# Performance work log

Measured on AMD Instinct MI355X. Metric: run time of the kernel, lower is better.

Reference implementation:

```python
import jax, jax.numpy as jnp
import numpy as np

B, NQ, NKV = 2, 2048, 2048
DIM, CTX_DIM = 1024, 1024
HEADS, DIM_HEAD = 16, 64
INNER = HEADS * DIM_HEAD  # 1024
SCALE = DIM_HEAD ** -0.5


def setup_inputs() -> dict:
    key = jax.random.key(0)
    ks = jax.random.split(key, 6)
    x = jax.random.normal(ks[0], (B, NQ, DIM), dtype=jnp.float32)
    context = jax.random.normal(ks[1], (B, NKV, CTX_DIM), dtype=jnp.float32)
    # nn.Linear weights stored as [out, in] in torch; we keep [in, out] for x @ W.
    Wq = jax.random.normal(ks[2], (DIM, INNER), dtype=jnp.float32) / np.sqrt(DIM)
    Wkv = jax.random.normal(ks[3], (CTX_DIM, 2 * INNER), dtype=jnp.float32) / np.sqrt(CTX_DIM)
    Wout = jax.random.normal(ks[4], (INNER, DIM), dtype=jnp.float32) / np.sqrt(INNER)
    bout = jax.random.normal(ks[5], (DIM,), dtype=jnp.float32) * 0.01
    return {"x": x, "context": context, "Wq": Wq, "Wkv": Wkv, "Wout": Wout, "bout": bout}


def reference(x, context, Wq, Wkv, Wout, bout):
    q = x @ Wq                      # [B, Nq, inner]
    kv = context @ Wkv              # [B, Nkv, 2*inner]
    k, v = jnp.split(kv, 2, axis=-1)

    def split_heads(t):             # [B, N, inner] -> [B, H, N, dh]
        return t.reshape(t.shape[0], t.shape[1], HEADS, DIM_HEAD).transpose(0, 2, 1, 3)

    q, k, v = split_heads(q), split_heads(k), split_heads(v)
    dots = jnp.einsum('bhqd,bhkd->bhqk', q, k) * SCALE  # [B, H, Nq, Nkv]
    attn = jax.nn.softmax(dots, axis=-1)
    out = jnp.einsum('bhqk,bhkd->bhqd', attn, v)        # [B, H, Nq, dh]
    out = out.transpose(0, 2, 1, 3).reshape(out.shape[0], out.shape[2], INNER)
    return out @ Wout + bout        # [B, Nq, dim]
```

## Files before the change

### kernel.cpp

```cpp
#include <hip/hip_runtime.h>
#include <hip/hip_bf16.h>
#include <stdint.h>

#define NQ 2048
#define NKV 2048
#define DIM 1024
#define INNER 1024
#define HEADS 16
#define DH 64
#define BATCH 2

typedef float f32x4 __attribute__((ext_vector_type(4)));
typedef float f32x16 __attribute__((ext_vector_type(16)));
typedef __bf16 bf16x8 __attribute__((ext_vector_type(8)));
typedef unsigned int u32x4 __attribute__((ext_vector_type(4)));

__device__ inline ushort f2b(float f) {
    uint32_t u = __builtin_bit_cast(uint32_t, f);
    u += 0x7fff + ((u >> 16) & 1);
    return (ushort)(u >> 16);
}

__device__ inline uint pkbf16(float lo, float hi) {
    __hip_bfloat162 h = __float22bfloat162_rn(make_float2(lo, hi));
    uint r;
    __builtin_memcpy(&r, &h, 4);
    return r;
}

__device__ __forceinline__ void gload16(const void* g, void* lds) {
    __builtin_amdgcn_global_load_lds(
        (const __attribute__((address_space(1))) unsigned int*)g,
        (__attribute__((address_space(3))) unsigned int*)lds, 16, 0, 0);
}

__global__ void prep(const float* __restrict__ x, const float* __restrict__ ctx,
                     const float* __restrict__ Wq, const float* __restrict__ Wkv,
                     const float* __restrict__ Wout,
                     ushort* __restrict__ xb, ushort* __restrict__ cb,
                     ushort* __restrict__ Wqt, ushort* __restrict__ Wkvt,
                     ushort* __restrict__ Woutt) {
    int z = blockIdx.z;
    if (z < 4) {
        __shared__ ushort tile[32][33];
        const float* src; ushort* dst; int C;
        if (z == 0)      { src = Wq;          dst = Wqt;                C = 1024; }
        else if (z == 1) { src = Wkv;         dst = Wkvt;               C = 2048; }
        else if (z == 2) { src = Wkv + 1024;  dst = Wkvt + 1024 * 1024; C = 2048; }
        else             { src = Wout;        dst = Woutt;              C = 1024; }
        int c0 = blockIdx.x * 32, r0 = blockIdx.y * 32;
        int tx = threadIdx.x, ty = threadIdx.y;
#pragma unroll
        for (int i = 0; i < 4; i++)
            tile[ty + i * 8][tx] = f2b(src[(size_t)(r0 + ty + i * 8) * C + c0 + tx]);
        __syncthreads();
#pragma unroll
        for (int i = 0; i < 4; i++)
            dst[(size_t)(c0 + ty + i * 8) * 1024 + r0 + tx] = tile[tx][ty + i * 8];
    } else {
        const int n4 = (BATCH * NQ * DIM) / 4;
        int fb = blockIdx.y * 32 + blockIdx.x;
        int t = threadIdx.y * 32 + threadIdx.x;
        for (int i = fb * 256 + t; i < 2 * n4; i += 1024 * 256) {
            float4 v;
            if (i < n4) v = ((const float4*)x)[i];
            else        v = ((const float4*)ctx)[i - n4];
            ushort4 o;
            o.x = f2b(v.x); o.y = f2b(v.y); o.z = f2b(v.z); o.w = f2b(v.w);
            if (i < n4) ((ushort4*)xb)[i] = o;
            else        ((ushort4*)cb)[i - n4] = o;
        }
    }
}

__global__ __launch_bounds__(256) void gemm_qkv(const ushort* __restrict__ xb, const ushort* __restrict__ cb,
                                                const ushort* __restrict__ Wqt, const ushort* __restrict__ Wkvt,
                                                ushort* __restrict__ qb, ushort* __restrict__ kb,
                                                ushort* __restrict__ vtb, float qscale) {
    constexpr int K = 1024, NT = 32;
    __shared__ ushort lds[24576];
    int flat = blockIdx.x;
    int swz = (flat & 7) * 96 + (flat >> 3);
    bool isq = swz < 256;
    const ushort *A, *Bt;
    int m0, n0;
    if (isq) { A = xb; Bt = Wqt;  m0 = (swz >> 3) * 128;  n0 = (swz & 7) * 128; }
    else     { int b2 = swz - 256; A = cb; Bt = Wkvt; m0 = (b2 >> 4) * 128; n0 = (b2 & 15) * 128; }
    int t = threadIdx.x, l = t & 63, w = t >> 6;
    int wr = w >> 1, wc = w & 1;
    int lg = l >> 4, lc = l & 15;
    f32x4 acc[4][4] = {};

    auto stage = [&](int buf, int k0) {
#pragma unroll
        for (int i = 0; i < 2; i++) {
            int s = w + i * 4;
            gload16(A + (size_t)(m0 + (s & 1) * 64 + l) * K + k0 + (s >> 1) * 8, &lds[buf * 8192 + s * 512]);
            gload16(Bt + (size_t)(n0 + (s & 1) * 64 + l) * K + k0 + (s >> 1) * 8, &lds[buf * 8192 + 4096 + s * 512]);
        }
    };

    stage(0, 0);
    stage(1, 32);
    for (int tt = 0; tt < NT; ++tt) {
        int cur = tt % 3;
        if (tt + 2 < NT) {
            stage((tt + 2) % 3, (tt + 2) * 32);
            asm volatile("s_waitcnt vmcnt(8)" ::: "memory");
        } else if (tt + 1 < NT) {
            asm volatile("s_waitcnt vmcnt(4)" ::: "memory");
        } else {
            asm volatile("s_waitcnt vmcnt(0)" ::: "memory");
        }
        __builtin_amdgcn_s_barrier();
        asm volatile("" ::: "memory");
        bf16x8 af[4], bf[4];
#pragma unroll
        for (int mi = 0; mi < 4; mi++)
            af[mi] = *(const bf16x8*)&lds[cur * 8192 + (lg * 128 + wr * 64 + mi * 16 + lc) * 8];
#pragma unroll
        for (int ni = 0; ni < 4; ni++)
            bf[ni] = *(const bf16x8*)&lds[cur * 8192 + 4096 + (lg * 128 + wc * 64 + ni * 16 + lc) * 8];
        __builtin_amdgcn_s_setprio(1);
#pragma unroll
        for (int mi = 0; mi < 4; mi++)
#pragma unroll
            for (int ni = 0; ni < 4; ni++)
                acc[mi][ni] = __builtin_amdgcn_mfma_f32_16x16x32_bf16(af[mi], bf[ni], acc[mi][ni], 0, 0, 0);
        __builtin_amdgcn_s_setprio(0);
        asm volatile("s_waitcnt lgkmcnt(0)" ::: "memory");
        __builtin_amdgcn_s_barrier();
        asm volatile("" ::: "memory");
    }
    if (isq) {
#pragma unroll
        for (int mi = 0; mi < 4; mi++)
#pragma unroll
            for (int ni = 0; ni < 4; ni++)
#pragma unroll
                for (int r = 0; r < 4; r++) {
                    int m = m0 + wr * 64 + mi * 16 + lg * 4 + r;
                    int n = n0 + wc * 64 + ni * 16 + lc;
                    qb[(size_t)m * 1024 + n] = f2b(acc[mi][ni][r] * qscale);
                }
    } else if (n0 < 1024) {
#pragma unroll
        for (int mi = 0; mi < 4; mi++)
#pragma unroll
            for (int ni = 0; ni < 4; ni++)
#pragma unroll
                for (int r = 0; r < 4; r++) {
                    int m = m0 + wr * 64 + mi * 16 + lg * 4 + r;
                    int n = n0 + wc * 64 + ni * 16 + lc;
                    kb[(size_t)m * 1024 + n] = f2b(acc[mi][ni][r]);
                }
    } else {
        int b = m0 >> 11, kv0 = m0 & 2047;
        int h0 = (n0 - 1024) >> 6;
#pragma unroll
        for (int mi = 0; mi < 4; mi++)
#pragma unroll
            for (int ni = 0; ni < 4; ni++)
#pragma unroll
                for (int r = 0; r < 4; r++) {
                    int ml = wr * 64 + mi * 16 + lg * 4 + r;
                    int nl = wc * 64 + ni * 16 + lc;
                    lds[nl * 136 + ml] = f2b(acc[mi][ni][r]);
                }
        __syncthreads();
#pragma unroll
        for (int c = 0; c < 8; c++) {
            int idx = c * 256 + t;
            int rrow = idx >> 4;
            int chunk = idx & 15;
            int h = h0 + (rrow >> 6), d = rrow & 63;
            u32x4 v = *(u32x4*)&lds[rrow * 136 + chunk * 8];
            *(u32x4*)&vtb[(((size_t)b * HEADS + h) * DH + d) * (size_t)NKV + kv0 + chunk * 8] = v;
        }
    }
}

__global__ __launch_bounds__(256) void gemm_out(const ushort* __restrict__ A, const ushort* __restrict__ Bt,
                                                float* __restrict__ C0, const float* __restrict__ bias) {
    constexpr int K = 1024, NT = 32;
    __shared__ ushort lds[24576];
    int flat = blockIdx.x;
    int swz = (flat & 7) * 32 + (flat >> 3);
    int m0 = (swz >> 3) * 128, n0 = (swz & 7) * 128;
    int t = threadIdx.x, l = t & 63, w = t >> 6;
    int wr = w >> 1, wc = w & 1;
    int lg = l >> 4, lc = l & 15;
    f32x4 acc[4][4] = {};

    auto stage = [&](int buf, int k0) {
#pragma unroll
        for (int i = 0; i < 2; i++) {
            int s = w + i * 4;
            gload16(A + (size_t)(m0 + (s & 1) * 64 + l) * K + k0 + (s >> 1) * 8, &lds[buf * 8192 + s * 512]);
            gload16(Bt + (size_t)(n0 + (s & 1) * 64 + l) * K + k0 + (s >> 1) * 8, &lds[buf * 8192 + 4096 + s * 512]);
        }
    };

    stage(0, 0);
    stage(1, 32);
    for (int tt = 0; tt < NT; ++tt) {
        int cur = tt % 3;
        if (tt + 2 < NT) {
            stage((tt + 2) % 3, (tt + 2) * 32);
            asm volatile("s_waitcnt vmcnt(8)" ::: "memory");
        } else if (tt + 1 < NT) {
            asm volatile("s_waitcnt vmcnt(4)" ::: "memory");
        } else {
            asm volatile("s_waitcnt vmcnt(0)" ::: "memory");
        }
        __builtin_amdgcn_s_barrier();
        asm volatile("" ::: "memory");
        bf16x8 af[4], bf[4];
#pragma unroll
        for (int mi = 0; mi < 4; mi++)
            af[mi] = *(const bf16x8*)&lds[cur * 8192 + (lg * 128 + wr * 64 + mi * 16 + lc) * 8];
#pragma unroll
        for (int ni = 0; ni < 4; ni++)
            bf[ni] = *(const bf16x8*)&lds[cur * 8192 + 4096 + (lg * 128 + wc * 64 + ni * 16 + lc) * 8];
        __builtin_amdgcn_s_setprio(1);
#pragma unroll
        for (int mi = 0; mi < 4; mi++)
#pragma unroll
            for (int ni = 0; ni < 4; ni++)
                acc[mi][ni] = __builtin_amdgcn_mfma_f32_16x16x32_bf16(af[mi], bf[ni], acc[mi][ni], 0, 0, 0);
        __builtin_amdgcn_s_setprio(0);
        asm volatile("s_waitcnt lgkmcnt(0)" ::: "memory");
        __builtin_amdgcn_s_barrier();
        asm volatile("" ::: "memory");
    }
#pragma unroll
    for (int mi = 0; mi < 4; mi++)
#pragma unroll
        for (int ni = 0; ni < 4; ni++)
#pragma unroll
            for (int r = 0; r < 4; r++) {
                int m = m0 + wr * 64 + mi * 16 + lg * 4 + r;
                int n = n0 + wc * 64 + ni * 16 + lc;
                C0[(size_t)m * 1024 + n] = acc[mi][ni][r] + bias[n];
            }
}

__global__ __launch_bounds__(256, 3) void attn9(const ushort* __restrict__ qb, const ushort* __restrict__ kb,
                                                const ushort* __restrict__ vtb, ushort* __restrict__ ob) {
    __shared__ ushort Ks[3][4096];
    __shared__ ushort Vs[3][4096];
    int flat = blockIdx.x;
    int swz = (flat & 7) * 64 + (flat >> 3);
    int qt = swz & 15, h = (swz >> 4) & 15, b = swz >> 8;
    int t = threadIdx.x, l = t & 63, w = t >> 6;
    int ll = l & 31, hi = l >> 5;
    const ushort* Qg = qb + (size_t)b * NQ * INNER + h * DH;
    const ushort* Kg = kb + (size_t)b * NKV * INNER + h * DH;
    const ushort* Vg = vtb + (((size_t)b * HEADS + h) * DH) * NKV;
    int q0 = qt * 128;
    constexpr int NT2 = NKV / 64;

    bf16x8 qf[4];
#pragma unroll
    for (int dchunk = 0; dchunk < 4; dchunk++) {
        int dc = dchunk * 2 + hi;
        qf[dchunk] = *(const bf16x8*)&Qg[(size_t)(q0 + w * 32 + ll) * INNER + dc * 8];
    }
    auto stageKV = [&](int buf, int kv0) {
#pragma unroll
        for (int i = 0; i < 2; i++) {
            int s = w + i * 4;
            gload16(Kg + (size_t)(kv0 + l) * INNER + s * 8, &Ks[buf][s * 512]);
            gload16(Vg + (size_t)l * NKV + kv0 + s * 8, &Vs[buf][s * 512]);
        }
    };
    stageKV(0, 0);
    stageKV(1, 64);

    f32x16 o0 = {}, o1 = {};
    float m_ = -1e30f, s_ = 0.f;
    f32x16 zf = {};

    for (int tt = 0; tt < NT2; ++tt) {
        int cur = tt % 3;
        if (tt == 0) {
            asm volatile("s_waitcnt vmcnt(4)" ::: "memory");
        } else if (tt + 1 < NT2) {
            asm volatile("s_waitcnt vmcnt(4)" ::: "memory");
        } else {
            asm volatile("s_waitcnt vmcnt(0)" ::: "memory");
        }
        __builtin_amdgcn_s_barrier();
        asm volatile("" ::: "memory");
        if (tt + 2 < NT2) stageKV((tt + 2) % 3, (tt + 2) * 64);

        f32x16 st0 = zf, st1 = zf;
        __builtin_amdgcn_s_setprio(1);
#pragma unroll
        for (int dchunk = 0; dchunk < 4; dchunk++) {
            int dc = dchunk * 2 + hi;
            bf16x8 kf0 = *(const bf16x8*)&Ks[cur][(dc * 64 + ll) * 8];
            bf16x8 kf1 = *(const bf16x8*)&Ks[cur][(dc * 64 + 32 + ll) * 8];
            st0 = __builtin_amdgcn_mfma_f32_32x32x16_bf16(kf0, qf[dchunk], st0, 0, 0, 0);
            st1 = __builtin_amdgcn_mfma_f32_32x32x16_bf16(kf1, qf[dchunk], st1, 0, 0, 0);
        }
        __builtin_amdgcn_s_setprio(0);

        float mx;
        {
            f32x16 m01 = __builtin_elementwise_max(st0, st1);
            float a = fmaxf(fmaxf(m01[0], m01[1]), fmaxf(m01[2], m01[3]));
            float b2 = fmaxf(fmaxf(m01[4], m01[5]), fmaxf(m01[6], m01[7]));
            float c = fmaxf(fmaxf(m01[8], m01[9]), fmaxf(m01[10], m01[11]));
            float d = fmaxf(fmaxf(m01[12], m01[13]), fmaxf(m01[14], m01[15]));
            mx = fmaxf(fmaxf(a, b2), fmaxf(c, d));
        }
        mx = fmaxf(mx, __shfl_xor(mx, 32));
        if (!__all(mx - m_ <= 8.f)) {
            float mn2 = fmaxf(m_, mx);
            float fac = __builtin_amdgcn_exp2f(m_ - mn2);
            m_ = mn2; s_ *= fac; o0 *= fac; o1 *= fac;
        }
        float mn = m_;
#pragma unroll
        for (int r = 0; r < 16; r++) st0[r] = __builtin_amdgcn_exp2f(st0[r] - mn);
#pragma unroll
        for (int r = 0; r < 16; r++) st1[r] = __builtin_amdgcn_exp2f(st1[r] - mn);
        float rs;
        {
            f32x16 sm = st0 + st1;
            float a = (sm[0] + sm[1]) + (sm[2] + sm[3]);
            float b2 = (sm[4] + sm[5]) + (sm[6] + sm[7]);
            float c = (sm[8] + sm[9]) + (sm[10] + sm[11]);
            float d = (sm[12] + sm[13]) + (sm[14] + sm[15]);
            rs = (a + b2) + (c + d);
        }
        rs += __shfl_xor(rs, 32);
        s_ += rs;

        bf16x8 pb[4];
#pragma unroll
        for (int kvb = 0; kvb < 2; kvb++)
#pragma unroll
            for (int c = 0; c < 2; c++) {
                int base = c * 8;
                const f32x16& s0 = (kvb == 0) ? st0 : st1;
                uint a0 = pkbf16(s0[base + 0], s0[base + 1]);
                uint a1 = pkbf16(s0[base + 2], s0[base + 3]);
                uint b0 = pkbf16(s0[base + 4], s0[base + 5]);
                uint b1 = pkbf16(s0[base + 6], s0[base + 7]);
                asm volatile("v_permlane32_swap_b32 %0, %1" : "+v"(a0), "+v"(b0));
                asm volatile("v_permlane32_swap_b32 %0, %1" : "+v"(a1), "+v"(b1));
                u32x4 wrd = {a0, a1, b0, b1};
                pb[kvb * 2 + c] = __builtin_bit_cast(bf16x8, wrd);
            }

        __builtin_amdgcn_s_setprio(1);
#pragma unroll
        for (int kvchunk = 0; kvchunk < 4; kvchunk++) {
            int kvc = kvchunk * 2 + hi;
            bf16x8 vf0 = *(const bf16x8*)&Vs[cur][(kvc * 64 + ll) * 8];
            bf16x8 vf1 = *(const bf16x8*)&Vs[cur][(kvc * 64 + 32 + ll) * 8];
            o0 = __builtin_amdgcn_mfma_f32_32x32x16_bf16(vf0, pb[kvchunk], o0, 0, 0, 0);
            o1 = __builtin_amdgcn_mfma_f32_32x32x16_bf16(vf1, pb[kvchunk], o1, 0, 0, 0);
        }
        __builtin_amdgcn_s_setprio(0);
    }

    ushort* Og = ob + (size_t)b * NQ * INNER + h * DH;
    float inv = 1.f / s_;
    int q = q0 + w * 32 + ll;
#pragma unroll
    for (int rq = 0; rq < 4; rq++) {
        int d0 = 8 * rq + 4 * hi;
        uint2 pw;
        pw.x = pkbf16(o0[4 * rq + 0] * inv, o0[4 * rq + 1] * inv);
        pw.y = pkbf16(o0[4 * rq + 2] * inv, o0[4 * rq + 3] * inv);
        *(uint2*)&Og[(size_t)q * INNER + d0] = pw;
        uint2 pw1;
        pw1.x = pkbf16(o1[4 * rq + 0] * inv, o1[4 * rq + 1] * inv);
        pw1.y = pkbf16(o1[4 * rq + 2] * inv, o1[4 * rq + 3] * inv);
        *(uint2*)&Og[(size_t)q * INNER + 32 + d0] = pw1;
    }
}

extern "C" void kernel_launch(void* const* d_in, const int* in_sizes, int n_in,
                              void* d_out, int out_size, void* d_ws, size_t ws_size,
                              hipStream_t stream) {
    const float* x    = (const float*)d_in[0];
    const float* ctx  = (const float*)d_in[1];
    const float* Wq   = (const float*)d_in[2];
    const float* Wkv  = (const float*)d_in[3];
    const float* Wout = (const float*)d_in[4];
    const float* bout = (const float*)d_in[5];
    float* out = (float*)d_out;

    if (ws_size < (size_t)(56u << 20)) return;
    char* ws = (char*)d_ws;
    ushort* xb    = (ushort*)(ws);
    ushort* cb    = (ushort*)(ws + (8u << 20));
    ushort* ob    = (ushort*)(ws + (8u << 20));
    ushort* qb    = (ushort*)(ws + (16u << 20));
    ushort* kb    = (ushort*)(ws + (24u << 20));
    ushort* vtb   = (ushort*)(ws + (32u << 20));
    ushort* Wqt   = (ushort*)(ws + (48u << 20));
    ushort* Wkvt  = (ushort*)(ws + (50u << 20));
    ushort* Woutt = (ushort*)(ws + (54u << 20));

    prep<<<dim3(32, 32, 5), dim3(32, 8), 0, stream>>>(x, ctx, Wq, Wkv, Wout, xb, cb, Wqt, Wkvt, Woutt);
    gemm_qkv<<<768, 256, 0, stream>>>(xb, cb, Wqt, Wkvt, qb, kb, vtb, 0.125f * 1.44269504f);
    attn9<<<512, 256, 0, stream>>>(qb, kb, vtb, ob);
    gemm_out<<<256, 256, 0, stream>>>(ob, Woutt, out, bout);
}
```

Before: 165.5 us.

## Enlarge QKV GEMM tile to 256x128 with 8 waves and swizzled V-transpose

```diff
diff --git a/kernel.cpp b/kernel.cpp
--- a/kernel.cpp
+++ b/kernel.cpp
@@ -73,30 +73,34 @@
     }
 }
 
-__global__ __launch_bounds__(256) void gemm_qkv(const ushort* __restrict__ xb, const ushort* __restrict__ cb,
-                                                const ushort* __restrict__ Wqt, const ushort* __restrict__ Wkvt,
-                                                ushort* __restrict__ qb, ushort* __restrict__ kb,
-                                                ushort* __restrict__ vtb, float qscale) {
+__global__ __launch_bounds__(512, 4) void gemm_qkv(const ushort* __restrict__ xb, const ushort* __restrict__ cb,
+                                                   const ushort* __restrict__ Wqt, const ushort* __restrict__ Wkvt,
+                                                   ushort* __restrict__ qb, ushort* __restrict__ kb,
+                                                   ushort* __restrict__ vtb, float qscale) {
     constexpr int K = 1024, NT = 32;
-    __shared__ ushort lds[24576];
+    __shared__ ushort lds[36864];
     int flat = blockIdx.x;
-    int swz = (flat & 7) * 96 + (flat >> 3);
-    bool isq = swz < 256;
+    int swz = (flat & 7) * 48 + (flat >> 3);
+    bool isq = swz < 128;
     const ushort *A, *Bt;
     int m0, n0;
-    if (isq) { A = xb; Bt = Wqt;  m0 = (swz >> 3) * 128;  n0 = (swz & 7) * 128; }
-    else     { int b2 = swz - 256; A = cb; Bt = Wkvt; m0 = (b2 >> 4) * 128; n0 = (b2 & 15) * 128; }
+    if (isq) { A = xb; Bt = Wqt;  m0 = (swz >> 3) * 256;  n0 = (swz & 7) * 128; }
+    else     { int b2 = swz - 128; A = cb; Bt = Wkvt; m0 = (b2 >> 4) * 256; n0 = (b2 & 15) * 128; }
     int t = threadIdx.x, l = t & 63, w = t >> 6;
-    int wr = w >> 1, wc = w & 1;
+    int wm = w >> 1, wn = w & 1;
     int lg = l >> 4, lc = l & 15;
     f32x4 acc[4][4] = {};
 
     auto stage = [&](int buf, int k0) {
 #pragma unroll
         for (int i = 0; i < 2; i++) {
-            int s = w + i * 4;
-            gload16(A + (size_t)(m0 + (s & 1) * 64 + l) * K + k0 + (s >> 1) * 8, &lds[buf * 8192 + s * 512]);
-            gload16(Bt + (size_t)(n0 + (s & 1) * 64 + l) * K + k0 + (s >> 1) * 8, &lds[buf * 8192 + 4096 + s * 512]);
+            int d = i * 8192 + t * 16;
+            int kc = d >> 12, row = (d >> 4) & 255;
+            gload16(A + (size_t)(m0 + row) * K + k0 + kc * 8, &lds[buf * 12288 + (d >> 1)]);
+        }
+        {
+            int kc = t >> 7, row = t & 127;
+            gload16(Bt + (size_t)(n0 + row) * K + k0 + kc * 8, &lds[buf * 12288 + 8192 + t * 8]);
         }
     };
 
@@ -106,9 +110,9 @@
         int cur = tt % 3;
         if (tt + 2 < NT) {
             stage((tt + 2) % 3, (tt + 2) * 32);
-            asm volatile("s_waitcnt vmcnt(8)" ::: "memory");
+            asm volatile("s_waitcnt vmcnt(6)" ::: "memory");
         } else if (tt + 1 < NT) {
-            asm volatile("s_waitcnt vmcnt(4)" ::: "memory");
+            asm volatile("s_waitcnt vmcnt(3)" ::: "memory");
         } else {
             asm volatile("s_waitcnt vmcnt(0)" ::: "memory");
         }
@@ -117,10 +121,10 @@
         bf16x8 af[4], bf[4];
 #pragma unroll
         for (int mi = 0; mi < 4; mi++)
-            af[mi] = *(const bf16x8*)&lds[cur * 8192 + (lg * 128 + wr * 64 + mi * 16 + lc) * 8];
+            af[mi] = *(const bf16x8*)&lds[cur * 12288 + (lg * 256 + wm * 64 + mi * 16 + lc) * 8];
 #pragma unroll
         for (int ni = 0; ni < 4; ni++)
-            bf[ni] = *(const bf16x8*)&lds[cur * 8192 + 4096 + (lg * 128 + wc * 64 + ni * 16 + lc) * 8];
+            bf[ni] = *(const bf16x8*)&lds[cur * 12288 + 8192 + (lg * 128 + wn * 64 + ni * 16 + lc) * 8];
         __builtin_amdgcn_s_setprio(1);
 #pragma unroll
         for (int mi = 0; mi < 4; mi++)
@@ -139,8 +143,8 @@
             for (int ni = 0; ni < 4; ni++)
 #pragma unroll
                 for (int r = 0; r < 4; r++) {
-                    int m = m0 + wr * 64 + mi * 16 + lg * 4 + r;
-                    int n = n0 + wc * 64 + ni * 16 + lc;
+                    int m = m0 + wm * 64 + mi * 16 + lg * 4 + r;
+                    int n = n0 + wn * 64 + ni * 16 + lc;
                     qb[(size_t)m * 1024 + n] = f2b(acc[mi][ni][r] * qscale);
                 }
     } else if (n0 < 1024) {
@@ -150,32 +154,32 @@
             for (int ni = 0; ni < 4; ni++)
 #pragma unroll
                 for (int r = 0; r < 4; r++) {
-                    int m = m0 + wr * 64 + mi * 16 + lg * 4 + r;
-                    int n = n0 + wc * 64 + ni * 16 + lc;
+                    int m = m0 + wm * 64 + mi * 16 + lg * 4 + r;
+                    int n = n0 + wn * 64 + ni * 16 + lc;
                     kb[(size_t)m * 1024 + n] = f2b(acc[mi][ni][r]);
                 }
     } else {
         int b = m0 >> 11, kv0 = m0 & 2047;
-        int h0 = (n0 - 1024) >> 6;
-#pragma unroll
-        for (int mi = 0; mi < 4; mi++)
-#pragma unroll
-            for (int ni = 0; ni < 4; ni++)
-#pragma unroll
-                for (int r = 0; r < 4; r++) {
-                    int ml = wr * 64 + mi * 16 + lg * 4 + r;
-                    int nl = wc * 64 + ni * 16 + lc;
-                    lds[nl * 136 + ml] = f2b(acc[mi][ni][r]);
-                }
+        int nb0 = n0 - 1024;
+#pragma unroll
+        for (int mi = 0; mi < 4; mi++)
+#pragma unroll
+            for (int ni = 0; ni < 4; ni++) {
+                int nl = wn * 64 + ni * 16 + lc;
+                int mlb = (wm * 64 + mi * 16 + lg * 4) ^ ((nl & 7) << 3);
+                ushort4 pk;
+                pk.x = f2b(acc[mi][ni][0]); pk.y = f2b(acc[mi][ni][1]);
+                pk.z = f2b(acc[mi][ni][2]); pk.w = f2b(acc[mi][ni][3]);
+                *(ushort4*)&lds[nl * 256 + mlb] = pk;
+            }
         __syncthreads();
 #pragma unroll
-        for (int c = 0; c < 8; c++) {
-            int idx = c * 256 + t;
-            int rrow = idx >> 4;
-            int chunk = idx & 15;
-            int h = h0 + (rrow >> 6), d = rrow & 63;
-            u32x4 v = *(u32x4*)&lds[rrow * 136 + chunk * 8];
-            *(u32x4*)&vtb[(((size_t)b * HEADS + h) * DH + d) * (size_t)NKV + kv0 + chunk * 8] = v;
+        for (int p = 0; p < 8; p++) {
+            int idx = p * 512 + t;
+            int nl = idx >> 5, mc = idx & 31;
+            u32x4 v = *(u32x4*)&lds[nl * 256 + (mc ^ (nl & 7)) * 8];
+            int h = (nb0 + nl) >> 6, d = (nb0 + nl) & 63;
+            *(u32x4*)&vtb[(((size_t)b * HEADS + h) * DH + d) * (size_t)NKV + kv0 + mc * 8] = v;
         }
     }
 }
@@ -283,9 +287,7 @@
 
     for (int tt = 0; tt < NT2; ++tt) {
         int cur = tt % 3;
-        if (tt == 0) {
-            asm volatile("s_waitcnt vmcnt(4)" ::: "memory");
-        } else if (tt + 1 < NT2) {
+        if (tt + 1 < NT2) {
             asm volatile("s_waitcnt vmcnt(4)" ::: "memory");
         } else {
             asm volatile("s_waitcnt vmcnt(0)" ::: "memory");
@@ -408,7 +410,7 @@
     ushort* Woutt = (ushort*)(ws + (54u << 20));
 
     prep<<<dim3(32, 32, 5), dim3(32, 8), 0, stream>>>(x, ctx, Wq, Wkv, Wout, xb, cb, Wqt, Wkvt, Woutt);
-    gemm_qkv<<<768, 256, 0, stream>>>(xb, cb, Wqt, Wkvt, qb, kb, vtb, 0.125f * 1.44269504f);
+    gemm_qkv<<<384, 512, 0, stream>>>(xb, cb, Wqt, Wkvt, qb, kb, vtb, 0.125f * 1.44269504f);
     attn9<<<512, 256, 0, stream>>>(qb, kb, vtb, ob);
     gemm_out<<<256, 256, 0, stream>>>(ob, Woutt, out, bout);
 }
```

Result: slower. 172.4 us (+4.2%).
